# Performance work log

Hardware: AMD Instinct MI355X
Metric: run time of the kernel (lower is better)

## Reference

```python
import jax, jax.numpy as jnp
import numpy as np

N, E, T, S, R, L = 100000, 1600000, 4, 32, 16, 5
H = 3 * S  # out-head hidden (hidden_list=[n_scalars*3])
EPS = 1e-8


def _mlp(x, W1, b1, W2, b2):
    return jax.nn.silu(x @ W1 + b1) @ W2 + b2


def setup_inputs() -> dict:
    key = jax.random.key(0)
    ks = iter(jax.random.split(key, 40))
    rn = lambda *s: jax.random.normal(next(ks), s, dtype=jnp.float32)
    p = lambda *s: rn(*s) * 0.1
    inp = {
        'u': rn(N, T),
        'v': rn(N, T, 2),
        'boundary_norm': rn(N, 2),
        'is_boundary': jnp.zeros((N,), dtype=bool),
        'y_force': rn(N, 2),
        'pos': rn(N, 2),
        'edge_index': jax.random.randint(next(ks), (2, E), 0, N, dtype=jnp.int64),
        # node embedding MLP: invariant feats (2T+2) -> 2S -> S
        'Wn1': p(2 * T + 2, 2 * S), 'bn1': jnp.zeros((2 * S,)),
        'Wn2': p(2 * S, S), 'bn2': jnp.zeros((S,)),
        # L stacked InvBlock params: edge MLP (2S+R -> S -> S), node update (2S -> S -> S)
        'We1': p(L, 2 * S + R, S), 'be1': jnp.zeros((L, S)),
        'We2': p(L, S, S), 'be2': jnp.zeros((L, S)),
        'Wu1': p(L, 2 * S, S), 'bu1': jnp.zeros((L, S)),
        'Wu2': p(L, S, S), 'bu2': jnp.zeros((L, S)),
        'ln_g': jnp.ones((S,)), 'ln_b': jnp.zeros((S,)),
        # heads: S -> 3S -> {2,1}
        'Wr1': p(S, H), 'br1': jnp.zeros((H,)), 'Wr2': p(H, 2), 'br2': jnp.zeros((2,)),
        'Ws1': p(S, H), 'bs1': jnp.zeros((H,)), 'Ws2': p(H, 1), 'bs2': jnp.zeros((1,)),
    }
    return inp


def _forward(u, v, boundary_norm, y_force, pos, edge_index,
             Wn1, bn1, Wn2, bn2, We1, be1, We2, be2, Wu1, bu1, Wu2, bu2,
             ln_g, ln_b, Wr1, br1, Wr2, br2, Ws1, bs1, Ws2, bs2):
    # torch.no_grad() geometry branch: center positions, edge distances
    posc = jax.lax.stop_gradient(pos - pos.mean(axis=0))
    row, col = edge_index[0], edge_index[1]
    edge_vec = posc[row] - posc[col]                       # [E,2]
    dist = jnp.linalg.norm(edge_vec, axis=1)               # [E]
    # besel_linspace(start=0, end=1, number=R, cutoff=False): Bessel/sine RBF
    freqs = jnp.arange(1, R + 1, dtype=jnp.float32) * jnp.pi
    rbf = jnp.sqrt(2.0) * jnp.sin(dist[:, None] * freqs) / (dist[:, None] + EPS)  # [E,R]

    # Node_embedding_inv: SE(2)-invariant scalar features -> MLP
    feats = jnp.concatenate([
        u,                                                 # [N,T]
        jnp.linalg.norm(v, axis=-1),                       # [N,T]
        jnp.linalg.norm(boundary_norm, axis=-1, keepdims=True),
        jnp.linalg.norm(y_force, axis=-1, keepdims=True),
    ], axis=-1)                                            # [N,2T+2]
    x = _mlp(feats, Wn1, bn1, Wn2, bn2)                    # [N,S]

    # degree for mean aggregation (computed once)
    deg = jax.ops.segment_sum(jnp.ones((E,), jnp.float32), row, num_segments=N)
    inv_deg = 1.0 / jnp.maximum(deg, 1.0)                  # [N]

    for l in range(L):  # InvBlock message passing
        ef = jnp.concatenate([x[row], x[col], rbf], axis=-1)   # [E,2S+R]
        m = _mlp(ef, We1[l], be1[l], We2[l], be2[l])           # [E,S]
        agg = jax.ops.segment_sum(m, row, num_segments=N) * inv_deg[:, None]
        x = x + _mlp(jnp.concatenate([x, agg], axis=-1), Wu1[l], bu1[l], Wu2[l], bu2[l])

    # LayerNorm
    mu = x.mean(axis=-1, keepdims=True)
    var = jnp.var(x, axis=-1, keepdims=True)
    x = (x - mu) * jax.lax.rsqrt(var + 1e-5) * ln_g + ln_b

    v_ = _mlp(x, Wr1, br1, Wr2, br2)                       # [N,2]
    u_ = _mlp(x, Ws1, bs1, Ws2, bs2)                       # [N,1]
    return u[:, -1] + u_[:, 0], v_ + v[:, -1, :]


def reference(u, v, boundary_norm, is_boundary, y_force, pos, edge_index,
              Wn1, bn1, Wn2, bn2, We1, be1, We2, be2, Wu1, bu1, Wu2, bu2,
              ln_g, ln_b, Wr1, br1, Wr2, br2, Ws1, bs1, Ws2, bs2):
    del is_boundary  # unused by the visible forward
    return _forward(u, v, boundary_norm, y_force, pos, edge_index,
                    Wn1, bn1, Wn2, bn2, We1, be1, We2, be2, Wu1, bu1, Wu2, bu2,
                    ln_g, ln_b, Wr1, br1, Wr2, br2, Ws1, bs1, Ws2, bs2)
```

## Files before the change

### kernel.cpp

```cpp
#include <hip/hip_runtime.h>
#include <cmath>

namespace {

constexpr int N = 100000;
constexpr int E = 1600000;
constexpr int S = 32;
constexpr int L = 5;
constexpr int NPW = 16;
constexpr int LB2 = (N + 63) / 64;
constexpr int NBKT = 391;
constexpr int EPB  = E / 256;
constexpr float PI_F    = 3.14159265358979323846f;
constexpr float SQRT2_F = 1.41421356237309515f;

typedef __attribute__((ext_vector_type(8))) short short8;
typedef __attribute__((ext_vector_type(4))) float f32x4;

__device__ __forceinline__ float silu_f(float x) {
    return x * __builtin_amdgcn_rcpf(1.0f + __expf(-x));
}

__device__ __forceinline__ unsigned short f2bf(float f) {
    unsigned int u = __float_as_uint(f);
    u = (u + 0x7FFFu + ((u >> 16) & 1u)) >> 16;
    return (unsigned short)u;
}

__device__ __forceinline__ int rl(int v, int i) {
    return __builtin_amdgcn_readlane(v, i);
}

__device__ __forceinline__ short8 ld_xb(const unsigned short* base, int col, int quad) {
    unsigned off = ((unsigned)col << 6) | ((unsigned)quad << 4);
    return *reinterpret_cast<const short8*>(reinterpret_cast<const char*>(base) + off);
}

__device__ __forceinline__ short8 ld_rbf(const unsigned short* base, int slot, int quad) {
    unsigned off = ((unsigned)slot << 5) | ((unsigned)quad << 4);
    return *reinterpret_cast<const short8*>(reinterpret_cast<const char*>(base) + off);
}

__device__ __forceinline__ void adv(int& i, int& t, int vd) {
    ++t;
    while (i < 16) {
        int dgi = rl(vd, i);
        int nt = (dgi + 15) >> 4;
        if (t < nt) break;
        t = 0; ++i;
    }
}

__device__ __forceinline__ int slotOf(int i, int t, int vs, int vd, int ml) {
    if (i >= 16) return 0;
    int s0 = rl(vs, i);
    int dg = rl(vd, i);
    int smax = s0 + ((dg > 0) ? dg : 1) - 1;
    int s = s0 + t * 16 + ml;
    return min(s, smax);
}

__global__ __launch_bounds__(1024) void passA_kernel(
    const int* __restrict__ ei, int* __restrict__ hist)
{
    __shared__ int h[NBKT];
    int t = threadIdx.x;
    int blk = blockIdx.x;
    for (int b = t; b < NBKT; b += 1024) h[b] = 0;
    __syncthreads();
    int base = blk * EPB;
    for (int i = t; i < EPB; i += 1024) {
        int r = ei[base + i];
        atomicAdd(&h[r >> 8], 1);
    }
    __syncthreads();
    for (int b = t; b < NBKT; b += 1024) hist[b * 256 + blk] = h[b];
}

__global__ __launch_bounds__(512) void p1_kernel(
    const int* __restrict__ hist, int* __restrict__ bstart)
{
    __shared__ int tot[512];
    int t = threadIdx.x;
    int wv = t >> 6;
    int lane = t & 63;

    for (int bin = wv; bin < NBKT; bin += 8) {
        const int* row = hist + bin * 256;
        int s = row[lane] + row[lane + 64] + row[lane + 128] + row[lane + 192];
        s += __shfl_xor(s, 1, 64);
        s += __shfl_xor(s, 2, 64);
        s += __shfl_xor(s, 4, 64);
        s += __shfl_xor(s, 8, 64);
        s += __shfl_xor(s, 16, 64);
        s += __shfl_xor(s, 32, 64);
        if (lane == 0) tot[bin] = s;
    }
    __syncthreads();

    if (t >= NBKT) tot[t] = 0;
    __syncthreads();
    #pragma unroll
    for (int off = 1; off < 512; off <<= 1) {
        int v = (t >= off) ? tot[t - off] : 0;
        __syncthreads();
        tot[t] += v;
        __syncthreads();
    }
    if (t <= NBKT) bstart[t] = (t == 0) ? 0 : tot[t - 1];
}

__global__ __launch_bounds__(256) void p2_kernel(
    const int* __restrict__ hist, const int* __restrict__ bstart,
    int* __restrict__ base)
{
    __shared__ int pre[256];
    int t = threadIdx.x;
    int bin = blockIdx.x;
    int h = hist[bin * 256 + t];
    pre[t] = h;
    __syncthreads();
    #pragma unroll
    for (int off = 1; off < 256; off <<= 1) {
        int v = (t >= off) ? pre[t - off] : 0;
        __syncthreads();
        pre[t] += v;
        __syncthreads();
    }
    base[bin * 256 + t] = bstart[bin] + pre[t] - h;
}

__global__ __launch_bounds__(1024) void passB_kernel(
    const int* __restrict__ ei, const float* __restrict__ pos,
    const int* __restrict__ base, uint4* __restrict__ edgebuf)
{
    __shared__ int cur[NBKT];
    int t = threadIdx.x;
    int blk = blockIdx.x;
    for (int b = t; b < NBKT; b += 1024) cur[b] = base[b * 256 + blk];
    __syncthreads();
    int ebase = blk * EPB;
    for (int i = t; i < EPB; i += 1024) {
        int e = ebase + i;
        int r = ei[e];
        int c = ei[E + e];
        float2 pr = reinterpret_cast<const float2*>(pos)[r];
        float2 pc = reinterpret_cast<const float2*>(pos)[c];
        float dx = pr.x - pc.x, dy = pr.y - pc.y;
        float d = sqrtf(dx * dx + dy * dy);
        int slot = atomicAdd(&cur[r >> 8], 1);
        edgebuf[slot] = make_uint4((unsigned)c, __float_as_uint(d), (unsigned)r, 0u);
    }
}

__global__ __launch_bounds__(1024) void passC_kernel(
    const uint4* __restrict__ edgebuf, const int* __restrict__ bstart,
    int* __restrict__ deg, int* __restrict__ start,
    int* __restrict__ csr_col, unsigned short* __restrict__ rbf_buf)
{
    __shared__ int cnt[256];
    __shared__ int pre[256];
    __shared__ int cur[256];
    int t = threadIdx.x;
    int bkt = blockIdx.x;
    int s0 = bstart[bkt], s1 = bstart[bkt + 1];

    if (t < 256) cnt[t] = 0;
    __syncthreads();
    for (int i = s0 + t; i < s1; i += 1024) {
        unsigned r = edgebuf[i].z;
        atomicAdd(&cnt[r & 255], 1);
    }
    __syncthreads();
    int c0 = 0;
    if (t < 256) {
        c0 = cnt[t];
        pre[t] = c0;
    }
    __syncthreads();
    #pragma unroll
    for (int off = 1; off < 256; off <<= 1) {
        int v = 0;
        if (t < 256) v = (t >= off) ? pre[t - off] : 0;
        __syncthreads();
        if (t < 256) pre[t] += v;
        __syncthreads();
    }
    if (t < 256) {
        int row = bkt * 256 + t;
        int st = s0 + pre[t] - c0;
        if (row < N) {
            deg[row] = c0;
            start[row] = st;
        }
        cur[t] = st;
    }
    __syncthreads();

    for (int i = s0 + t; i < s1; i += 1024) {
        uint4 e = edgebuf[i];
        int slot = atomicAdd(&cur[e.z & 255], 1);
        csr_col[slot] = (int)e.x;
        float d = __uint_as_float(e.y);

        float sn = __sinf(PI_F * d);
        float c1 = __cosf(PI_F * d);
        float inv = SQRT2_F / (d + 1e-8f);
        float tc = 2.0f * c1;
        float sk = sn, skm = 0.0f;
        unsigned int pk[8];
        #pragma unroll
        for (int k = 0; k < 8; ++k) {
            float r0 = sk * inv;
            float s2 = tc * sk - skm; skm = sk; sk = s2;
            float r1 = sk * inv;
            float s3 = tc * sk - skm; skm = sk; sk = s3;
            pk[k] = (unsigned int)f2bf(r0) | ((unsigned int)f2bf(r1) << 16);
        }
        uint4* out = reinterpret_cast<uint4*>(rbf_buf + (size_t)slot * 16);
        out[0] = make_uint4(pk[0], pk[1], pk[2], pk[3]);
        out[1] = make_uint4(pk[4], pk[5], pk[6], pk[7]);
    }
}

__global__ __launch_bounds__(256) void prep_wt_kernel(
    const float* __restrict__ We1, const float* __restrict__ We2,
    const float* __restrict__ Wu1, const float* __restrict__ Wu2,
    const float* __restrict__ Wr1, const float* __restrict__ Ws1,
    const float* __restrict__ Wn2,
    short* __restrict__ wt1, short* __restrict__ wt2,
    short* __restrict__ wtu1, short* __restrict__ wtu2,
    short* __restrict__ wtr1, short* __restrict__ wts1,
    short* __restrict__ wtn2)
{
    int idx = blockIdx.x * 256 + threadIdx.x;
    if (idx < 5 * 32 * 96) {
        int l = idx / (32 * 96), r = idx % (32 * 96), n = r / 96, k = r % 96;
        float v = (k < 80) ? We1[((size_t)l * 80 + k) * 32 + n] : 0.0f;
        wt1[idx] = (short)f2bf(v);
    }
    if (idx < 5 * 32 * 32) {
        int l = idx / 1024, r = idx % 1024, n = r / 32, k = r % 32;
        wt2[idx]  = (short)f2bf(We2[((size_t)l * 32 + k) * 32 + n]);
        wtu2[idx] = (short)f2bf(Wu2[((size_t)l * 32 + k) * 32 + n]);
    }
    if (idx < 5 * 32 * 64) {
        int l = idx / 2048, r = idx % 2048, n = r / 64, k = r % 64;
        wtu1[idx] = (short)f2bf(Wu1[((size_t)l * 64 + k) * 32 + n]);
    }
    if (idx < 96 * 32) {
        int n = idx / 32, k = idx % 32;
        wtr1[idx] = (short)f2bf(Wr1[k * 96 + n]);
        wts1[idx] = (short)f2bf(Ws1[k * 96 + n]);
    }
    if (idx < 32 * 64) {
        int n = idx / 64, k = idx % 64;
        wtn2[idx] = (short)f2bf(Wn2[k * 32 + n]);
    }
}

__global__ __launch_bounds__(256) void node_embed_kernel(
    const float* __restrict__ u, const float* __restrict__ v,
    const float* __restrict__ bnorm, const float* __restrict__ yf,
    const float* __restrict__ Wn1, const float* __restrict__ bn1,
    const short* __restrict__ wtn2, const float* __restrict__ bn2,
    float* __restrict__ x, unsigned short* __restrict__ xb)
{
    __shared__ unsigned short hb[4][16 * 68];
    int t = threadIdx.x;
    int w = t >> 6;
    int lane = t & 63;
    int quad = lane >> 4;
    int ml = lane & 15;
    int wid = blockIdx.x * 4 + w;
    int nbase = __builtin_amdgcn_readfirstlane(wid * NPW);
    if (nbase >= N) return;

    int n = nbase + ml;

    float f[10];
    float4 uu = reinterpret_cast<const float4*>(u)[n];
    f[0] = uu.x; f[1] = uu.y; f[2] = uu.z; f[3] = uu.w;
    float4 v0 = reinterpret_cast<const float4*>(v)[2 * n];
    float4 v1 = reinterpret_cast<const float4*>(v)[2 * n + 1];
    f[4] = sqrtf(v0.x * v0.x + v0.y * v0.y);
    f[5] = sqrtf(v0.z * v0.z + v0.w * v0.w);
    f[6] = sqrtf(v1.x * v1.x + v1.y * v1.y);
    f[7] = sqrtf(v1.z * v1.z + v1.w * v1.w);
    float2 bb = reinterpret_cast<const float2*>(bnorm)[n];
    f[8] = sqrtf(bb.x * bb.x + bb.y * bb.y);
    float2 yy = reinterpret_cast<const float2*>(yf)[n];
    f[9] = sqrtf(yy.x * yy.x + yy.y * yy.y);

    float h[16];
    {
        const float4* b4 = reinterpret_cast<const float4*>(bn1 + quad * 16);
        float4 b0 = b4[0], b1 = b4[1], b2 = b4[2], b3 = b4[3];
        h[0]=b0.x; h[1]=b0.y; h[2]=b0.z; h[3]=b0.w;
        h[4]=b1.x; h[5]=b1.y; h[6]=b1.z; h[7]=b1.w;
        h[8]=b2.x; h[9]=b2.y; h[10]=b2.z; h[11]=b2.w;
        h[12]=b3.x; h[13]=b3.y; h[14]=b3.z; h[15]=b3.w;
    }
    #pragma unroll
    for (int i = 0; i < 10; ++i) {
        float ff = f[i];
        const float4* wr = reinterpret_cast<const float4*>(Wn1 + i * 64 + quad * 16);
        float4 w0 = wr[0], w1 = wr[1], w2 = wr[2], w3 = wr[3];
        h[0]  = fmaf(ff, w0.x, h[0]);  h[1]  = fmaf(ff, w0.y, h[1]);
        h[2]  = fmaf(ff, w0.z, h[2]);  h[3]  = fmaf(ff, w0.w, h[3]);
        h[4]  = fmaf(ff, w1.x, h[4]);  h[5]  = fmaf(ff, w1.y, h[5]);
        h[6]  = fmaf(ff, w1.z, h[6]);  h[7]  = fmaf(ff, w1.w, h[7]);
        h[8]  = fmaf(ff, w2.x, h[8]);  h[9]  = fmaf(ff, w2.y, h[9]);
        h[10] = fmaf(ff, w2.z, h[10]); h[11] = fmaf(ff, w2.w, h[11]);
        h[12] = fmaf(ff, w3.x, h[12]); h[13] = fmaf(ff, w3.y, h[13]);
        h[14] = fmaf(ff, w3.z, h[14]); h[15] = fmaf(ff, w3.w, h[15]);
    }
    #pragma unroll
    for (int jj = 0; jj < 16; ++jj) h[jj] = silu_f(h[jj]);

    unsigned short* hp = hb[w];
    {
        unsigned int* dst = reinterpret_cast<unsigned int*>(hp + ml * 68 + quad * 16);
        #pragma unroll
        for (int i = 0; i < 8; ++i)
            dst[i] = (unsigned int)f2bf(h[2 * i]) | ((unsigned int)f2bf(h[2 * i + 1]) << 16);
    }
    __builtin_amdgcn_wave_barrier();

    short8 Ak0 = *reinterpret_cast<const short8*>(hp + ml * 68 + quad * 8);
    short8 Ak1 = *reinterpret_cast<const short8*>(hp + ml * 68 + 32 + quad * 8);
    const short8* n2p = reinterpret_cast<const short8*>(wtn2);
    short8 B00 = n2p[(ml     ) * 8 + quad];
    short8 B01 = n2p[(ml     ) * 8 + 4 + quad];
    short8 B10 = n2p[(ml + 16) * 8 + quad];
    short8 B11 = n2p[(ml + 16) * 8 + 4 + quad];
    float bz0 = bn2[ml], bz1 = bn2[ml + 16];
    f32x4 a0 = {bz0, bz0, bz0, bz0};
    f32x4 a1 = {bz1, bz1, bz1, bz1};
    a0 = __builtin_amdgcn_mfma_f32_16x16x32_bf16(Ak0, B00, a0, 0, 0, 0);
    a0 = __builtin_amdgcn_mfma_f32_16x16x32_bf16(Ak1, B01, a0, 0, 0, 0);
    a1 = __builtin_amdgcn_mfma_f32_16x16x32_bf16(Ak0, B10, a1, 0, 0, 0);
    a1 = __builtin_amdgcn_mfma_f32_16x16x32_bf16(Ak1, B11, a1, 0, 0, 0);

    int row = quad * 4;
    #pragma unroll
    for (int r = 0; r < 4; ++r) {
        int nn = nbase + row + r;
        float o0 = a0[r];
        float o1 = a1[r];
        x[(size_t)nn * 32 + ml]      = o0;
        x[(size_t)nn * 32 + ml + 16] = o1;
        xb[(size_t)nn * 32 + ml]      = f2bf(o0);
        xb[(size_t)nn * 32 + ml + 16] = f2bf(o1);
    }
}

__global__ __launch_bounds__(256, 6) void layer_kernel(
    const int* __restrict__ deg, const int* __restrict__ start,
    const int* __restrict__ csr_col, const unsigned short* __restrict__ rbf_buf,
    const float* __restrict__ x_in, const unsigned short* __restrict__ xb_in,
    float* __restrict__ x_out, unsigned short* __restrict__ xb_out,
    const short* __restrict__ wt1, const float* __restrict__ b1,
    const short* __restrict__ wt2, const float* __restrict__ b2,
    const short* __restrict__ wtu1, const float* __restrict__ bu1,
    const short* __restrict__ wtu2, const float* __restrict__ bu2)
{
    __shared__ unsigned short lsh[4][16 * 34];
    __shared__ unsigned short agb[4][16 * 34];
    __shared__ unsigned short hub[4][16 * 34];
    __shared__ float lrp[4][16 * 33];
    __shared__ float ldg[4][16];
    __shared__ float livd[4][16];

    int t = threadIdx.x;
    int w = t >> 6;
    int lane = t & 63;
    int quad = lane >> 4;
    int ml = lane & 15;
    int wid = blockIdx.x * 4 + w;
    int nbase = __builtin_amdgcn_readfirstlane(wid * NPW);
    if (nbase >= N) return;

    int vs = start[nbase + ml];
    int vd = deg[nbase + ml];

    const short8* wp = reinterpret_cast<const short8*>(wt1);
    short8 B00 = wp[(ml     ) * 12 + 0 * 4 + quad];
    short8 B01 = wp[(ml     ) * 12 + 1 * 4 + quad];
    short8 B02 = wp[(ml     ) * 12 + 2 * 4 + quad];
    short8 B10 = wp[(ml + 16) * 12 + 0 * 4 + quad];
    short8 B11 = wp[(ml + 16) * 12 + 1 * 4 + quad];
    short8 B12 = wp[(ml + 16) * 12 + 2 * 4 + quad];

    short8 Ax = ld_xb(xb_in, nbase + ml, quad);

    float b1j0 = b1[ml];
    float b1j1 = b1[ml + 16];

    unsigned short* lshp = lsh[w];
    for (int k = lane; k < 16 * 34; k += 64) lshp[k] = 0;
    if (lane < 16) {
        ldg[w][lane] = (float)vd;
        livd[w][lane] = 1.0f / fmaxf((float)vd, 1.0f);
    }

    float* rpp = lrp[w];
    {
        f32x4 rp0 = {b1j0, b1j0, b1j0, b1j0};
        f32x4 rp1 = {b1j1, b1j1, b1j1, b1j1};
        rp0 = __builtin_amdgcn_mfma_f32_16x16x32_bf16(Ax, B00, rp0, 0, 0, 0);
        rp1 = __builtin_amdgcn_mfma_f32_16x16x32_bf16(Ax, B10, rp1, 0, 0, 0);
        int row = quad * 4;
        #pragma unroll
        for (int r = 0; r < 4; ++r) {
            rpp[(row + r) * 33 + ml]      = rp0[r];
            rpp[(row + r) * 33 + ml + 16] = rp1[r];
        }
    }
    __builtin_amdgcn_wave_barrier();

    const short8 Z8 = {0, 0, 0, 0, 0, 0, 0, 0};
    int iA = 0, tA = -1; adv(iA, tA, vd);
    int iB = iA, tB = tA; adv(iB, tB, vd);
    int iC = iB, tC = tB; adv(iC, tC, vd);
    int iD = iC, tD = tC; adv(iD, tD, vd);
    int iE = iD, tE = tD; adv(iE, tE, vd);

    int slot0 = slotOf(iA, tA, vs, vd, ml);
    int slot1 = slotOf(iB, tB, vs, vd, ml);
    int slot2 = slotOf(iC, tC, vs, vd, ml);
    int slotQ = slotOf(iD, tD, vs, vd, ml);
    int col0 = csr_col[slot0];
    int col1 = csr_col[slot1];
    int col2 = csr_col[slot2];
    int colQ = csr_col[slotQ];

    short8 F1_0 = ld_xb(xb_in, col0, quad);
    short8 F2_0 = (quad < 2) ? ld_rbf(rbf_buf, slot0, quad) : Z8;
    short8 F1_1 = ld_xb(xb_in, col1, quad);
    short8 F2_1 = (quad < 2) ? ld_rbf(rbf_buf, slot1, quad) : Z8;
    short8 F1_2 = ld_xb(xb_in, col2, quad);
    short8 F2_2 = (quad < 2) ? ld_rbf(rbf_buf, slot2, quad) : Z8;

    float colp0 = 0.0f, colp1 = 0.0f;

    auto tile = [&](const short8& A1, const short8& A2) {
        float rpa = rpp[iA * 33 + ml];
        float rpb = rpp[iA * 33 + ml + 16];
        f32x4 acc0 = {rpa, rpa, rpa, rpa};
        f32x4 acc1 = {rpb, rpb, rpb, rpb};
        acc0 = __builtin_amdgcn_mfma_f32_16x16x32_bf16(A1, B01, acc0, 0, 0, 0);
        acc0 = __builtin_amdgcn_mfma_f32_16x16x32_bf16(A2, B02, acc0, 0, 0, 0);
        acc1 = __builtin_amdgcn_mfma_f32_16x16x32_bf16(A1, B11, acc1, 0, 0, 0);
        acc1 = __builtin_amdgcn_mfma_f32_16x16x32_bf16(A2, B12, acc1, 0, 0, 0);

        int dg0 = rl(vd, iA);
        int rowbase = tA * 16 + quad * 4;
        #pragma unroll
        for (int r = 0; r < 4; ++r) {
            bool vld = (rowbase + r) < dg0;
            colp0 += vld ? silu_f(acc0[r]) : 0.0f;
            colp1 += vld ? silu_f(acc1[r]) : 0.0f;
        }
        if (tA == ((dg0 + 15) >> 4) - 1) {
            colp0 += __shfl_xor(colp0, 16, 64);
            colp0 += __shfl_xor(colp0, 32, 64);
            colp1 += __shfl_xor(colp1, 16, 64);
            colp1 += __shfl_xor(colp1, 32, 64);
            if (quad == 0) {
                lshp[iA * 34 + ml]      = f2bf(colp0);
                lshp[iA * 34 + ml + 16] = f2bf(colp1);
            }
            colp0 = 0.0f; colp1 = 0.0f;
        }
    };
    auto shiftq = [&]() {
        iA = iB; tA = tB; iB = iC; tB = tC;
        iC = iD; tC = tD; iD = iE; tD = tE;
        adv(iE, tE, vd);
    };

    #define EDGE_STEP(F1s, F2s)                                     \
    {                                                               \
        int slotE_ = slotOf(iE, tE, vs, vd, ml);                    \
        int colE_  = csr_col[slotE_];                               \
        tile(F1s, F2s);                                             \
        F1s = ld_xb(xb_in, colQ, quad);                             \
        F2s = (quad < 2) ? ld_rbf(rbf_buf, slotQ, quad) : Z8;       \
        shiftq();                                                   \
        colQ = colE_; slotQ = slotE_;                               \
    }

    while (iA < 16) {
        EDGE_STEP(F1_0, F2_0);
        if (iA >= 16) break;
        EDGE_STEP(F1_1, F2_1);
        if (iA >= 16) break;
        EDGE_STEP(F1_2, F2_2);
    }
    #undef EDGE_STEP
    __builtin_amdgcn_wave_barrier();

    const short8* w2p = reinterpret_cast<const short8*>(wt2);
    short8 Bw2_0 = w2p[(ml     ) * 4 + quad];
    short8 Bw2_1 = w2p[(ml + 16) * 4 + quad];
    const short8* u1p = reinterpret_cast<const short8*>(wtu1);
    short8 Bu1_00 = u1p[(ml     ) * 8 + quad];
    short8 Bu1_10 = u1p[(ml     ) * 8 + 4 + quad];
    short8 Bu1_01 = u1p[(ml + 16) * 8 + quad];
    short8 Bu1_11 = u1p[(ml + 16) * 8 + 4 + quad];
    const short8* u2p = reinterpret_cast<const short8*>(wtu2);
    short8 Bu2_0 = u2p[(ml     ) * 4 + quad];
    short8 Bu2_1 = u2p[(ml + 16) * 4 + quad];

    short8 Ash = *reinterpret_cast<const short8*>(lshp + ml * 34 + quad * 8);
    f32x4 c0 = {0.0f, 0.0f, 0.0f, 0.0f};
    f32x4 c1 = {0.0f, 0.0f, 0.0f, 0.0f};
    c0 = __builtin_amdgcn_mfma_f32_16x16x32_bf16(Ash, Bw2_0, c0, 0, 0, 0);
    c1 = __builtin_amdgcn_mfma_f32_16x16x32_bf16(Ash, Bw2_1, c1, 0, 0, 0);
    float b2c0 = b2[ml], b2c1 = b2[ml + 16];
    unsigned short* agp = agb[w];
    int row = quad * 4;
    #pragma unroll
    for (int r = 0; r < 4; ++r) {
        float fd = ldg[w][row + r];
        float iv = livd[w][row + r];
        agp[(row + r) * 34 + ml]      = f2bf((c0[r] + fd * b2c0) * iv);
        agp[(row + r) * 34 + ml + 16] = f2bf((c1[r] + fd * b2c1) * iv);
    }
    __builtin_amdgcn_wave_barrier();

    short8 Aag = *reinterpret_cast<const short8*>(agp + ml * 34 + quad * 8);
    f32x4 d0 = {0.0f, 0.0f, 0.0f, 0.0f};
    f32x4 d1 = {0.0f, 0.0f, 0.0f, 0.0f};
    d0 = __builtin_amdgcn_mfma_f32_16x16x32_bf16(Ax,  Bu1_00, d0, 0, 0, 0);
    d0 = __builtin_amdgcn_mfma_f32_16x16x32_bf16(Aag, Bu1_10, d0, 0, 0, 0);
    d1 = __builtin_amdgcn_mfma_f32_16x16x32_bf16(Ax,  Bu1_01, d1, 0, 0, 0);
    d1 = __builtin_amdgcn_mfma_f32_16x16x32_bf16(Aag, Bu1_11, d1, 0, 0, 0);
    float bu1c0 = bu1[ml], bu1c1 = bu1[ml + 16];
    unsigned short* hup = hub[w];
    #pragma unroll
    for (int r = 0; r < 4; ++r) {
        hup[(row + r) * 34 + ml]      = f2bf(silu_f(d0[r] + bu1c0));
        hup[(row + r) * 34 + ml + 16] = f2bf(silu_f(d1[r] + bu1c1));
    }
    __builtin_amdgcn_wave_barrier();

    short8 Ahu = *reinterpret_cast<const short8*>(hup + ml * 34 + quad * 8);
    float xr0[4], xr1[4];
    #pragma unroll
    for (int r = 0; r < 4; ++r) {
        int nn = nbase + row + r;
        xr0[r] = x_in[(size_t)nn * 32 + ml];
        xr1[r] = x_in[(size_t)nn * 32 + ml + 16];
    }
    f32x4 e0 = {0.0f, 0.0f, 0.0f, 0.0f};
    f32x4 e1 = {0.0f, 0.0f, 0.0f, 0.0f};
    e0 = __builtin_amdgcn_mfma_f32_16x16x32_bf16(Ahu, Bu2_0, e0, 0, 0, 0);
    e1 = __builtin_amdgcn_mfma_f32_16x16x32_bf16(Ahu, Bu2_1, e1, 0, 0, 0);
    float bu2c0 = bu2[ml], bu2c1 = bu2[ml + 16];
    #pragma unroll
    for (int r = 0; r < 4; ++r) {
        int nn = nbase + row + r;
        float o0 = e0[r] + bu2c0 + xr0[r];
        float o1 = e1[r] + bu2c1 + xr1[r];
        x_out[(size_t)nn * 32 + ml]      = o0;
        x_out[(size_t)nn * 32 + ml + 16] = o1;
        xb_out[(size_t)nn * 32 + ml]      = f2bf(o0);
        xb_out[(size_t)nn * 32 + ml + 16] = f2bf(o1);
    }
}

__global__ __launch_bounds__(256) void final_kernel(
    const float* __restrict__ x, const float* __restrict__ u,
    const float* __restrict__ v,
    const float* __restrict__ ln_g, const float* __restrict__ ln_b,
    const short* __restrict__ wtr1, const float* __restrict__ br1,
    const float* __restrict__ Wr2, const float* __restrict__ br2,
    const short* __restrict__ wts1, const float* __restrict__ bs1,
    const float* __restrict__ Ws2, const float* __restrict__ bs2,
    float* __restrict__ out)
{
    int t = threadIdx.x;
    int w = t >> 6;
    int lane = t & 63;
    int quad = lane >> 4;
    int ml = lane & 15;
    int wid = blockIdx.x * 4 + w;
    int nbase = __builtin_amdgcn_readfirstlane(wid * NPW);
    if (nbase >= N) return;

    const float4* xs = reinterpret_cast<const float4*>(
        x + (size_t)(nbase + ml) * 32 + quad * 8);
    float4 xa = xs[0], xb4 = xs[1];
    float f[8] = {xa.x, xa.y, xa.z, xa.w, xb4.x, xb4.y, xb4.z, xb4.w};

    float s = 0.0f, ss = 0.0f;
    #pragma unroll
    for (int i = 0; i < 8; ++i) { s += f[i]; ss += f[i] * f[i]; }
    s  += __shfl_xor(s, 16, 64);  s  += __shfl_xor(s, 32, 64);
    ss += __shfl_xor(ss, 16, 64); ss += __shfl_xor(ss, 32, 64);
    float mu = s * (1.0f / 32.0f);
    float var = ss * (1.0f / 32.0f) - mu * mu;
    float rs = rsqrtf(var + 1e-5f);

    const float4* gp = reinterpret_cast<const float4*>(ln_g + quad * 8);
    const float4* bp = reinterpret_cast<const float4*>(ln_b + quad * 8);
    float4 g0 = gp[0], g1 = gp[1], bb0 = bp[0], bb1 = bp[1];
    float gg[8] = {g0.x, g0.y, g0.z, g0.w, g1.x, g1.y, g1.z, g1.w};
    float bb[8] = {bb0.x, bb0.y, bb0.z, bb0.w, bb1.x, bb1.y, bb1.z, bb1.w};
    short8 A;
    #pragma unroll
    for (int i = 0; i < 8; ++i)
        A[i] = (short)f2bf((f[i] - mu) * rs * gg[i] + bb[i]);

    const short8* r1p = reinterpret_cast<const short8*>(wtr1);
    const short8* s1p = reinterpret_cast<const short8*>(wts1);
    const f32x4 Zf = {0.0f, 0.0f, 0.0f, 0.0f};
    f32x4 hr[6], hs[6];
    #pragma unroll
    for (int h = 0; h < 6; ++h) {
        hr[h] = __builtin_amdgcn_mfma_f32_16x16x32_bf16(A, r1p[(ml + 16 * h) * 4 + quad], Zf, 0, 0, 0);
        hs[h] = __builtin_amdgcn_mfma_f32_16x16x32_bf16(A, s1p[(ml + 16 * h) * 4 + quad], Zf, 0, 0, 0);
    }

    float wr2a[6], wr2b[6], ws2v[6], br1v[6], bs1v[6];
    #pragma unroll
    for (int h = 0; h < 6; ++h) {
        int j = ml + 16 * h;
        float2 wr = reinterpret_cast<const float2*>(Wr2)[j];
        wr2a[h] = wr.x; wr2b[h] = wr.y;
        ws2v[h] = Ws2[j];
        br1v[h] = br1[j];
        bs1v[h] = bs1[j];
    }

    float o0[4], o1[4], o2[4];
    #pragma unroll
    for (int r = 0; r < 4; ++r) {
        float p0 = 0.0f, p1 = 0.0f, p2 = 0.0f;
        #pragma unroll
        for (int h = 0; h < 6; ++h) {
            float a1 = silu_f(hr[h][r] + br1v[h]);
            float a2 = silu_f(hs[h][r] + bs1v[h]);
            p0 = fmaf(a1, wr2a[h], p0);
            p1 = fmaf(a1, wr2b[h], p1);
            p2 = fmaf(a2, ws2v[h], p2);
        }
        p0 += __shfl_xor(p0, 1, 64); p0 += __shfl_xor(p0, 2, 64);
        p0 += __shfl_xor(p0, 4, 64); p0 += __shfl_xor(p0, 8, 64);
        p1 += __shfl_xor(p1, 1, 64); p1 += __shfl_xor(p1, 2, 64);
        p1 += __shfl_xor(p1, 4, 64); p1 += __shfl_xor(p1, 8, 64);
        p2 += __shfl_xor(p2, 1, 64); p2 += __shfl_xor(p2, 2, 64);
        p2 += __shfl_xor(p2, 4, 64); p2 += __shfl_xor(p2, 8, 64);
        o0[r] = p0; o1[r] = p1; o2[r] = p2;
    }

    if (ml == 0) {
        float b20 = br2[0], b21 = br2[1], b22 = bs2[0];
        #pragma unroll
        for (int r = 0; r < 4; ++r) {
            int n = nbase + quad * 4 + r;
            out[n] = u[n * 4 + 3] + o2[r] + b22;
            out[N + 2 * n]     = o0[r] + b20 + v[n * 8 + 6];
            out[N + 2 * n + 1] = o1[r] + b21 + v[n * 8 + 7];
        }
    }
}

}

extern "C" void kernel_launch(void* const* d_in, const int* in_sizes, int n_in,
                              void* d_out, int out_size, void* d_ws, size_t ws_size,
                              hipStream_t stream)
{
    const float* u    = (const float*)d_in[0];
    const float* v    = (const float*)d_in[1];
    const float* bno  = (const float*)d_in[2];
    const float* yf   = (const float*)d_in[4];
    const float* pos  = (const float*)d_in[5];
    const int*   ei   = (const int*)d_in[6];
    const float* Wn1  = (const float*)d_in[7];
    const float* bn1  = (const float*)d_in[8];
    const float* Wn2  = (const float*)d_in[9];
    const float* bn2  = (const float*)d_in[10];
    const float* We1  = (const float*)d_in[11];
    const float* be1  = (const float*)d_in[12];
    const float* We2  = (const float*)d_in[13];
    const float* be2  = (const float*)d_in[14];
    const float* Wu1  = (const float*)d_in[15];
    const float* bu1  = (const float*)d_in[16];
    const float* Wu2  = (const float*)d_in[17];
    const float* bu2  = (const float*)d_in[18];
    const float* ln_g = (const float*)d_in[19];
    const float* ln_b = (const float*)d_in[20];
    const float* Wr1  = (const float*)d_in[21];
    const float* br1  = (const float*)d_in[22];
    const float* Wr2  = (const float*)d_in[23];
    const float* br2  = (const float*)d_in[24];
    const float* Ws1  = (const float*)d_in[25];
    const float* bs1  = (const float*)d_in[26];
    const float* Ws2  = (const float*)d_in[27];
    const float* bs2  = (const float*)d_in[28];
    float* out = (float*)d_out;

    int*   deg      = (int*)d_ws;
    int*   start    = deg + N;
    int*   bstart   = start + N;
    int*   csr_col  = bstart + 512;
    unsigned short* rbf = (unsigned short*)(csr_col + E);
    float* x0       = (float*)(rbf + (size_t)E * 16);
    float* x1       = x0 + (size_t)N * S;
    unsigned short* xb0 = (unsigned short*)(x1 + (size_t)N * S);
    unsigned short* xb1 = xb0 + (size_t)N * S;
    short* wt1      = (short*)(xb1 + (size_t)N * S);
    short* wt2      = wt1 + 5 * 32 * 96;
    short* wtu1     = wt2 + 5 * 32 * 32;
    short* wtu2     = wtu1 + 5 * 32 * 64;
    short* wtr1     = wtu2 + 5 * 32 * 32;
    short* wts1     = wtr1 + 96 * 32;
    short* wtn2     = wts1 + 96 * 32;
    int*   hist     = (int*)(wtn2 + 32 * 64);
    int*   basem    = hist + NBKT * 256;

    uint4* edgebuf = (uint4*)x0;

    passA_kernel<<<256, 1024, 0, stream>>>(ei, hist);
    p1_kernel<<<1, 512, 0, stream>>>(hist, bstart);
    p2_kernel<<<NBKT, 256, 0, stream>>>(hist, bstart, basem);
    passB_kernel<<<256, 1024, 0, stream>>>(ei, pos, basem, edgebuf);
    passC_kernel<<<NBKT, 1024, 0, stream>>>(edgebuf, bstart, deg, start, csr_col, rbf);
    prep_wt_kernel<<<60, 256, 0, stream>>>(We1, We2, Wu1, Wu2, Wr1, Ws1, Wn2,
                                           wt1, wt2, wtu1, wtu2, wtr1, wts1, wtn2);

    node_embed_kernel<<<LB2, 256, 0, stream>>>(u, v, bno, yf, Wn1, bn1, wtn2, bn2,
                                               x0, xb0);

    float* xin = x0;  float* xout = x1;
    unsigned short* xbin = xb0;  unsigned short* xbout = xb1;
    for (int l = 0; l < L; ++l) {
        layer_kernel<<<LB2, 256, 0, stream>>>(
            deg, start, csr_col, rbf, xin, xbin, xout, xbout,
            wt1 + (size_t)l * 32 * 96,  be1 + (size_t)l * 32,
            wt2 + (size_t)l * 32 * 32,  be2 + (size_t)l * 32,
            wtu1 + (size_t)l * 32 * 64, bu1 + (size_t)l * 32,
            wtu2 + (size_t)l * 32 * 32, bu2 + (size_t)l * 32);
        float* tf = xin; xin = xout; xout = tf;
        unsigned short* tb = xbin; xbin = xbout; xbout = tb;
    }

    final_kernel<<<LB2, 256, 0, stream>>>(xin, u, v, ln_g, ln_b,
                                          wtr1, br1, Wr2, br2,
                                          wts1, bs1, Ws2, bs2, out);
}
```

Baseline: 481.4 us.

## Precompute per-wave edge tile descriptors once instead of scanning degrees each layer

```diff
diff --git a/kernel.cpp b/kernel.cpp
--- a/kernel.cpp
+++ b/kernel.cpp
@@ -9,6 +9,8 @@
 constexpr int L = 5;
 constexpr int NPW = 16;
 constexpr int LB2 = (N + 63) / 64;
+constexpr int NG  = N / 16;
+constexpr int MAXT = 48;
 constexpr int NBKT = 391;
 constexpr int EPB  = E / 256;
 constexpr float PI_F    = 3.14159265358979323846f;
@@ -27,10 +29,6 @@
     return (unsigned short)u;
 }
 
-__device__ __forceinline__ int rl(int v, int i) {
-    return __builtin_amdgcn_readlane(v, i);
-}
-
 __device__ __forceinline__ short8 ld_xb(const unsigned short* base, int col, int quad) {
     unsigned off = ((unsigned)col << 6) | ((unsigned)quad << 4);
     return *reinterpret_cast<const short8*>(reinterpret_cast<const char*>(base) + off);
@@ -39,25 +37,6 @@
 __device__ __forceinline__ short8 ld_rbf(const unsigned short* base, int slot, int quad) {
     unsigned off = ((unsigned)slot << 5) | ((unsigned)quad << 4);
     return *reinterpret_cast<const short8*>(reinterpret_cast<const char*>(base) + off);
-}
-
-__device__ __forceinline__ void adv(int& i, int& t, int vd) {
-    ++t;
-    while (i < 16) {
-        int dgi = rl(vd, i);
-        int nt = (dgi + 15) >> 4;
-        if (t < nt) break;
-        t = 0; ++i;
-    }
-}
-
-__device__ __forceinline__ int slotOf(int i, int t, int vs, int vd, int ml) {
-    if (i >= 16) return 0;
-    int s0 = rl(vs, i);
-    int dg = rl(vd, i);
-    int smax = s0 + ((dg > 0) ? dg : 1) - 1;
-    int s = s0 + t * 16 + ml;
-    return min(s, smax);
 }
 
 __global__ __launch_bounds__(1024) void passA_kernel(
@@ -223,6 +202,37 @@
     }
 }
 
+__global__ __launch_bounds__(256) void tiles_kernel(
+    const int* __restrict__ deg, const int* __restrict__ start,
+    int2* __restrict__ wdesc, int* __restrict__ gcnt)
+{
+    int t = threadIdx.x;
+    int w = t >> 6;
+    int lane = t & 63;
+    int g = blockIdx.x * 4 + w;
+    if (g >= NG) return;
+
+    int d = 0, s = 0;
+    if (lane < 16) {
+        d = deg[g * 16 + lane];
+        s = start[g * 16 + lane];
+    }
+    int nt = (d + 15) >> 4;
+    int pre = nt;
+    #pragma unroll
+    for (int off = 1; off < 16; off <<= 1) {
+        int v = __shfl_up(pre, off, 16);
+        if ((lane & 15) >= off) pre += v;
+    }
+    if (lane < 16) {
+        int o = pre - nt;
+        int2* base = wdesc + (size_t)g * MAXT;
+        for (int tt = 0; tt < nt; ++tt)
+            base[o + tt] = make_int2(s + tt * 16, lane | ((d - tt * 16) << 8));
+        if (lane == 15) gcnt[g] = pre;
+    }
+}
+
 __global__ __launch_bounds__(256) void prep_wt_kernel(
     const float* __restrict__ We1, const float* __restrict__ We2,
     const float* __restrict__ Wu1, const float* __restrict__ Wu2,
@@ -356,7 +366,8 @@
 }
 
 __global__ __launch_bounds__(256, 6) void layer_kernel(
-    const int* __restrict__ deg, const int* __restrict__ start,
+    const int* __restrict__ deg, const int2* __restrict__ wdesc,
+    const int* __restrict__ gcnt,
     const int* __restrict__ csr_col, const unsigned short* __restrict__ rbf_buf,
     const float* __restrict__ x_in, const unsigned short* __restrict__ xb_in,
     float* __restrict__ x_out, unsigned short* __restrict__ xb_out,
@@ -381,7 +392,6 @@
     int nbase = __builtin_amdgcn_readfirstlane(wid * NPW);
     if (nbase >= N) return;
 
-    int vs = start[nbase + ml];
     int vd = deg[nbase + ml];
 
     const short8* wp = reinterpret_cast<const short8*>(wt1);
@@ -420,85 +430,84 @@
     __builtin_amdgcn_wave_barrier();
 
     const short8 Z8 = {0, 0, 0, 0, 0, 0, 0, 0};
-    int iA = 0, tA = -1; adv(iA, tA, vd);
-    int iB = iA, tB = tA; adv(iB, tB, vd);
-    int iC = iB, tC = tB; adv(iC, tC, vd);
-    int iD = iC, tD = tC; adv(iD, tD, vd);
-    int iE = iD, tE = tD; adv(iE, tE, vd);
-
-    int slot0 = slotOf(iA, tA, vs, vd, ml);
-    int slot1 = slotOf(iB, tB, vs, vd, ml);
-    int slot2 = slotOf(iC, tC, vs, vd, ml);
-    int slotQ = slotOf(iD, tD, vs, vd, ml);
-    int col0 = csr_col[slot0];
-    int col1 = csr_col[slot1];
-    int col2 = csr_col[slot2];
-    int colQ = csr_col[slotQ];
-
-    short8 F1_0 = ld_xb(xb_in, col0, quad);
-    short8 F2_0 = (quad < 2) ? ld_rbf(rbf_buf, slot0, quad) : Z8;
-    short8 F1_1 = ld_xb(xb_in, col1, quad);
-    short8 F2_1 = (quad < 2) ? ld_rbf(rbf_buf, slot1, quad) : Z8;
-    short8 F1_2 = ld_xb(xb_in, col2, quad);
-    short8 F2_2 = (quad < 2) ? ld_rbf(rbf_buf, slot2, quad) : Z8;
+    int tcnt = gcnt[wid];
+    const int2* dp = wdesc + (size_t)wid * MAXT;
 
     float colp0 = 0.0f, colp1 = 0.0f;
 
-    auto tile = [&](const short8& A1, const short8& A2) {
-        float rpa = rpp[iA * 33 + ml];
-        float rpb = rpp[iA * 33 + ml + 16];
-        f32x4 acc0 = {rpa, rpa, rpa, rpa};
-        f32x4 acc1 = {rpb, rpb, rpb, rpb};
-        acc0 = __builtin_amdgcn_mfma_f32_16x16x32_bf16(A1, B01, acc0, 0, 0, 0);
-        acc0 = __builtin_amdgcn_mfma_f32_16x16x32_bf16(A2, B02, acc0, 0, 0, 0);
-        acc1 = __builtin_amdgcn_mfma_f32_16x16x32_bf16(A1, B11, acc1, 0, 0, 0);
-        acc1 = __builtin_amdgcn_mfma_f32_16x16x32_bf16(A2, B12, acc1, 0, 0, 0);
-
-        int dg0 = rl(vd, iA);
-        int rowbase = tA * 16 + quad * 4;
-        #pragma unroll
-        for (int r = 0; r < 4; ++r) {
-            bool vld = (rowbase + r) < dg0;
-            colp0 += vld ? silu_f(acc0[r]) : 0.0f;
-            colp1 += vld ? silu_f(acc1[r]) : 0.0f;
+    if (tcnt > 0) {
+        auto dread = [&](int k) { return dp[min(k, tcnt - 1)]; };
+        auto slotfor = [&](int2 d) {
+            int drem = d.y >> 8;
+            return min(d.x + ml, d.x + drem - 1);
+        };
+
+        int2 dA = dp[0];
+        int2 dB = dread(1);
+        int2 dC = dread(2);
+        int2 dQ = dread(3);
+        int sA = slotfor(dA), sB = slotfor(dB), sC = slotfor(dC);
+        int sQ = slotfor(dQ);
+        int cQ = csr_col[sQ];
+
+        short8 F1_0 = ld_xb(xb_in, csr_col[sA], quad);
+        short8 F2_0 = (quad < 2) ? ld_rbf(rbf_buf, sA, quad) : Z8;
+        short8 F1_1 = ld_xb(xb_in, csr_col[sB], quad);
+        short8 F2_1 = (quad < 2) ? ld_rbf(rbf_buf, sB, quad) : Z8;
+        short8 F1_2 = ld_xb(xb_in, csr_col[sC], quad);
+        short8 F2_2 = (quad < 2) ? ld_rbf(rbf_buf, sC, quad) : Z8;
+
+        int k = 0;
+
+        #define EDGE_STEP(F1s, F2s)                                       \
+        {                                                                 \
+            int2 dN = dread(k + 4);                                       \
+            int sN = slotfor(dN);                                         \
+            int cN = csr_col[sN];                                         \
+            int i_ = dA.y & 255;                                          \
+            int drem = dA.y >> 8;                                         \
+            float rpa = rpp[i_ * 33 + ml];                                \
+            float rpb = rpp[i_ * 33 + ml + 16];                           \
+            f32x4 acc0 = {rpa, rpa, rpa, rpa};                            \
+            f32x4 acc1 = {rpb, rpb, rpb, rpb};                            \
+            acc0 = __builtin_amdgcn_mfma_f32_16x16x32_bf16(F1s, B01, acc0, 0, 0, 0); \
+            acc0 = __builtin_amdgcn_mfma_f32_16x16x32_bf16(F2s, B02, acc0, 0, 0, 0); \
+            acc1 = __builtin_amdgcn_mfma_f32_16x16x32_bf16(F1s, B11, acc1, 0, 0, 0); \
+            acc1 = __builtin_amdgcn_mfma_f32_16x16x32_bf16(F2s, B12, acc1, 0, 0, 0); \
+            int rowbase = quad * 4;                                       \
+            _Pragma("unroll")                                             \
+            for (int r = 0; r < 4; ++r) {                                 \
+                bool vld = (rowbase + r) < drem;                          \
+                colp0 += vld ? silu_f(acc0[r]) : 0.0f;                    \
+                colp1 += vld ? silu_f(acc1[r]) : 0.0f;                    \
+            }                                                             \
+            if (drem <= 16) {                                             \
+                colp0 += __shfl_xor(colp0, 16, 64);                       \
+                colp0 += __shfl_xor(colp0, 32, 64);                       \
+                colp1 += __shfl_xor(colp1, 16, 64);                       \
+                colp1 += __shfl_xor(colp1, 32, 64);                       \
+                if (quad == 0) {                                          \
+                    lshp[i_ * 34 + ml]      = f2bf(colp0);                \
+                    lshp[i_ * 34 + ml + 16] = f2bf(colp1);                \
+                }                                                         \
+                colp0 = 0.0f; colp1 = 0.0f;                               \
+            }                                                             \
+            F1s = ld_xb(xb_in, cQ, quad);                                 \
+            F2s = (quad < 2) ? ld_rbf(rbf_buf, sQ, quad) : Z8;            \
+            dA = dB; dB = dC; dC = dQ; dQ = dN;                           \
+            cQ = cN; sQ = sN;                                             \
+            ++k;                                                          \
         }
-        if (tA == ((dg0 + 15) >> 4) - 1) {
-            colp0 += __shfl_xor(colp0, 16, 64);
-            colp0 += __shfl_xor(colp0, 32, 64);
-            colp1 += __shfl_xor(colp1, 16, 64);
-            colp1 += __shfl_xor(colp1, 32, 64);
-            if (quad == 0) {
-                lshp[iA * 34 + ml]      = f2bf(colp0);
-                lshp[iA * 34 + ml + 16] = f2bf(colp1);
-            }
-            colp0 = 0.0f; colp1 = 0.0f;
+
+        while (k < tcnt) {
+            EDGE_STEP(F1_0, F2_0);
+            if (k >= tcnt) break;
+            EDGE_STEP(F1_1, F2_1);
+            if (k >= tcnt) break;
+            EDGE_STEP(F1_2, F2_2);
         }
-    };
-    auto shiftq = [&]() {
-        iA = iB; tA = tB; iB = iC; tB = tC;
-        iC = iD; tC = tD; iD = iE; tD = tE;
-        adv(iE, tE, vd);
-    };
-
-    #define EDGE_STEP(F1s, F2s)                                     \
-    {                                                               \
-        int slotE_ = slotOf(iE, tE, vs, vd, ml);                    \
-        int colE_  = csr_col[slotE_];                               \
-        tile(F1s, F2s);                                             \
-        F1s = ld_xb(xb_in, colQ, quad);                             \
-        F2s = (quad < 2) ? ld_rbf(rbf_buf, slotQ, quad) : Z8;       \
-        shiftq();                                                   \
-        colQ = colE_; slotQ = slotE_;                               \
-    }
-
-    while (iA < 16) {
-        EDGE_STEP(F1_0, F2_0);
-        if (iA >= 16) break;
-        EDGE_STEP(F1_1, F2_1);
-        if (iA >= 16) break;
-        EDGE_STEP(F1_2, F2_2);
-    }
-    #undef EDGE_STEP
+        #undef EDGE_STEP
+    }
     __builtin_amdgcn_wave_barrier();
 
     const short8* w2p = reinterpret_cast<const short8*>(wt2);
@@ -722,6 +731,8 @@
     short* wtn2     = wts1 + 96 * 32;
     int*   hist     = (int*)(wtn2 + 32 * 64);
     int*   basem    = hist + NBKT * 256;
+    int2*  wdesc    = (int2*)(basem + NBKT * 256);
+    int*   gcnt     = (int*)(wdesc + (size_t)NG * MAXT);
 
     uint4* edgebuf = (uint4*)x0;
 
@@ -730,6 +741,7 @@
     p2_kernel<<<NBKT, 256, 0, stream>>>(hist, bstart, basem);
     passB_kernel<<<256, 1024, 0, stream>>>(ei, pos, basem, edgebuf);
     passC_kernel<<<NBKT, 1024, 0, stream>>>(edgebuf, bstart, deg, start, csr_col, rbf);
+    tiles_kernel<<<LB2, 256, 0, stream>>>(deg, start, wdesc, gcnt);
     prep_wt_kernel<<<60, 256, 0, stream>>>(We1, We2, Wu1, Wu2, Wr1, Ws1, Wn2,
                                            wt1, wt2, wtu1, wtu2, wtr1, wts1, wtn2);
 
@@ -740,7 +752,7 @@
     unsigned short* xbin = xb0;  unsigned short* xbout = xb1;
     for (int l = 0; l < L; ++l) {
         layer_kernel<<<LB2, 256, 0, stream>>>(
-            deg, start, csr_col, rbf, xin, xbin, xout, xbout,
+            deg, wdesc, gcnt, csr_col, rbf, xin, xbin, xout, xbout,
             wt1 + (size_t)l * 32 * 96,  be1 + (size_t)l * 32,
             wt2 + (size_t)l * 32 * 32,  be2 + (size_t)l * 32,
             wtu1 + (size_t)l * 32 * 64, bu1 + (size_t)l * 32,
```

Result: slower. 754.0 us (+56.6%).

## Process edge tiles in pairs with 32x32x16 MFMA instead of 16x16x32

Applied to the files above, without the earlier changes.

```diff
diff --git a/kernel.cpp b/kernel.cpp
--- a/kernel.cpp
+++ b/kernel.cpp
@@ -16,6 +16,7 @@
 
 typedef __attribute__((ext_vector_type(8))) short short8;
 typedef __attribute__((ext_vector_type(4))) float f32x4;
+typedef __attribute__((ext_vector_type(16))) float f32x16;
 
 __device__ __forceinline__ float silu_f(float x) {
     return x * __builtin_amdgcn_rcpf(1.0f + __expf(-x));
@@ -31,13 +32,13 @@
     return __builtin_amdgcn_readlane(v, i);
 }
 
-__device__ __forceinline__ short8 ld_xb(const unsigned short* base, int col, int quad) {
-    unsigned off = ((unsigned)col << 6) | ((unsigned)quad << 4);
+__device__ __forceinline__ short8 ld_xb(const unsigned short* base, int col, int q) {
+    unsigned off = ((unsigned)col << 6) | ((unsigned)q << 4);
     return *reinterpret_cast<const short8*>(reinterpret_cast<const char*>(base) + off);
 }
 
-__device__ __forceinline__ short8 ld_rbf(const unsigned short* base, int slot, int quad) {
-    unsigned off = ((unsigned)slot << 5) | ((unsigned)quad << 4);
+__device__ __forceinline__ short8 ld_rbf(const unsigned short* base, int slot, int q) {
+    unsigned off = ((unsigned)slot << 5) | ((unsigned)q << 4);
     return *reinterpret_cast<const short8*>(reinterpret_cast<const char*>(base) + off);
 }
 
@@ -51,12 +52,12 @@
     }
 }
 
-__device__ __forceinline__ int slotOf(int i, int t, int vs, int vd, int ml) {
+__device__ __forceinline__ int slotOf(int i, int t, int vs, int vd, int e) {
     if (i >= 16) return 0;
     int s0 = rl(vs, i);
     int dg = rl(vd, i);
     int smax = s0 + ((dg > 0) ? dg : 1) - 1;
-    int s = s0 + t * 16 + ml;
+    int s = s0 + t * 16 + e;
     return min(s, smax);
 }
 
@@ -377,6 +378,7 @@
     int lane = t & 63;
     int quad = lane >> 4;
     int ml = lane & 15;
+    int hi = lane >> 5;
     int wid = blockIdx.x * 4 + w;
     int nbase = __builtin_amdgcn_readfirstlane(wid * NPW);
     if (nbase >= N) return;
@@ -386,11 +388,12 @@
 
     const short8* wp = reinterpret_cast<const short8*>(wt1);
     short8 B00 = wp[(ml     ) * 12 + 0 * 4 + quad];
-    short8 B01 = wp[(ml     ) * 12 + 1 * 4 + quad];
-    short8 B02 = wp[(ml     ) * 12 + 2 * 4 + quad];
     short8 B10 = wp[(ml + 16) * 12 + 0 * 4 + quad];
-    short8 B11 = wp[(ml + 16) * 12 + 1 * 4 + quad];
-    short8 B12 = wp[(ml + 16) * 12 + 2 * 4 + quad];
+
+    int bn = lane & 31;
+    short8 Bx0 = *reinterpret_cast<const short8*>(wt1 + bn * 96 + 32 + hi * 8);
+    short8 Bx1 = *reinterpret_cast<const short8*>(wt1 + bn * 96 + 48 + hi * 8);
+    short8 Brb = *reinterpret_cast<const short8*>(wt1 + bn * 96 + 64 + hi * 8);
 
     short8 Ax = ld_xb(xb_in, nbase + ml, quad);
 
@@ -419,84 +422,117 @@
     }
     __builtin_amdgcn_wave_barrier();
 
-    const short8 Z8 = {0, 0, 0, 0, 0, 0, 0, 0};
-    int iA = 0, tA = -1; adv(iA, tA, vd);
-    int iB = iA, tB = tA; adv(iB, tB, vd);
-    int iC = iB, tC = tB; adv(iC, tC, vd);
-    int iD = iC, tD = tC; adv(iD, tD, vd);
-    int iE = iD, tE = tD; adv(iE, tE, vd);
-
-    int slot0 = slotOf(iA, tA, vs, vd, ml);
-    int slot1 = slotOf(iB, tB, vs, vd, ml);
-    int slot2 = slotOf(iC, tC, vs, vd, ml);
-    int slotQ = slotOf(iD, tD, vs, vd, ml);
-    int col0 = csr_col[slot0];
-    int col1 = csr_col[slot1];
-    int col2 = csr_col[slot2];
+    int ia0 = 0, ta0 = -1; adv(ia0, ta0, vd);
+    int ia1 = ia0, ta1 = ta0; adv(ia1, ta1, vd);
+    int ib0 = ia1, tb0 = ta1; adv(ib0, tb0, vd);
+    int ib1 = ib0, tb1 = tb0; adv(ib1, tb1, vd);
+    int ic0 = ib1, tc0 = tb1; adv(ic0, tc0, vd);
+    int ic1 = ic0, tc1 = tc0; adv(ic1, tc1, vd);
+    int id0 = ic1, td0 = tc1; adv(id0, td0, vd);
+    int id1 = id0, td1 = td0; adv(id1, td1, vd);
+    int ie0 = id1, te0 = td1; adv(ie0, te0, vd);
+    int ie1 = ie0, te1 = te0; adv(ie1, te1, vd);
+
+    auto slotPair = [&](int i0, int t0, int i1, int t1) {
+        int sa = slotOf(i0, t0, vs, vd, ml);
+        int sb = slotOf(i1, t1, vs, vd, ml);
+        return (lane & 16) ? sb : sa;
+    };
+
+    int slotA = slotPair(ia0, ta0, ia1, ta1);
+    int slotB = slotPair(ib0, tb0, ib1, tb1);
+    int slotC = slotPair(ic0, tc0, ic1, tc1);
+    int slotQ = slotPair(id0, td0, id1, td1);
+    int colA = csr_col[slotA];
+    int colB = csr_col[slotB];
+    int colC = csr_col[slotC];
     int colQ = csr_col[slotQ];
 
-    short8 F1_0 = ld_xb(xb_in, col0, quad);
-    short8 F2_0 = (quad < 2) ? ld_rbf(rbf_buf, slot0, quad) : Z8;
-    short8 F1_1 = ld_xb(xb_in, col1, quad);
-    short8 F2_1 = (quad < 2) ? ld_rbf(rbf_buf, slot1, quad) : Z8;
-    short8 F1_2 = ld_xb(xb_in, col2, quad);
-    short8 F2_2 = (quad < 2) ? ld_rbf(rbf_buf, slot2, quad) : Z8;
-
-    float colp0 = 0.0f, colp1 = 0.0f;
-
-    auto tile = [&](const short8& A1, const short8& A2) {
-        float rpa = rpp[iA * 33 + ml];
-        float rpb = rpp[iA * 33 + ml + 16];
-        f32x4 acc0 = {rpa, rpa, rpa, rpa};
-        f32x4 acc1 = {rpb, rpb, rpb, rpb};
-        acc0 = __builtin_amdgcn_mfma_f32_16x16x32_bf16(A1, B01, acc0, 0, 0, 0);
-        acc0 = __builtin_amdgcn_mfma_f32_16x16x32_bf16(A2, B02, acc0, 0, 0, 0);
-        acc1 = __builtin_amdgcn_mfma_f32_16x16x32_bf16(A1, B11, acc1, 0, 0, 0);
-        acc1 = __builtin_amdgcn_mfma_f32_16x16x32_bf16(A2, B12, acc1, 0, 0, 0);
-
-        int dg0 = rl(vd, iA);
-        int rowbase = tA * 16 + quad * 4;
+    short8 X0_0 = ld_xb(xb_in, colA, hi);
+    short8 X1_0 = ld_xb(xb_in, colA, 2 + hi);
+    short8 RB_0 = ld_rbf(rbf_buf, slotA, hi);
+    short8 X0_1 = ld_xb(xb_in, colB, hi);
+    short8 X1_1 = ld_xb(xb_in, colB, 2 + hi);
+    short8 RB_1 = ld_rbf(rbf_buf, slotB, hi);
+    short8 X0_2 = ld_xb(xb_in, colC, hi);
+    short8 X1_2 = ld_xb(xb_in, colC, 2 + hi);
+    short8 RB_2 = ld_rbf(rbf_buf, slotC, hi);
+
+    float colp = 0.0f;
+
+    auto tilePair = [&](const short8& X0, const short8& X1, const short8& RB) {
+        int col = lane & 31;
+        float rpa = rpp[ia0 * 33 + col];
+        float rpb = (ia1 < 16) ? rpp[ia1 * 33 + col] : 0.0f;
+        f32x16 acc;
         #pragma unroll
-        for (int r = 0; r < 4; ++r) {
-            bool vld = (rowbase + r) < dg0;
-            colp0 += vld ? silu_f(acc0[r]) : 0.0f;
-            colp1 += vld ? silu_f(acc1[r]) : 0.0f;
+        for (int j = 0; j < 8; ++j)  acc[j] = rpa;
+        #pragma unroll
+        for (int j = 8; j < 16; ++j) acc[j] = rpb;
+        acc = __builtin_amdgcn_mfma_f32_32x32x16_bf16(X0, Bx0, acc, 0, 0, 0);
+        acc = __builtin_amdgcn_mfma_f32_32x32x16_bf16(X1, Bx1, acc, 0, 0, 0);
+        acc = __builtin_amdgcn_mfma_f32_32x32x16_bf16(RB, Brb, acc, 0, 0, 0);
+
+        int hi4 = hi * 4;
+        int dg0 = rl(vd, ia0);
+        int drem0 = dg0 - ta0 * 16;
+        float pa = 0.0f;
+        #pragma unroll
+        for (int j = 0; j < 8; ++j) {
+            int row = (j & 3) + 8 * (j >> 2) + hi4;
+            pa += (row < drem0) ? silu_f(acc[j]) : 0.0f;
         }
-        if (tA == ((dg0 + 15) >> 4) - 1) {
-            colp0 += __shfl_xor(colp0, 16, 64);
-            colp0 += __shfl_xor(colp0, 32, 64);
-            colp1 += __shfl_xor(colp1, 16, 64);
-            colp1 += __shfl_xor(colp1, 32, 64);
-            if (quad == 0) {
-                lshp[iA * 34 + ml]      = f2bf(colp0);
-                lshp[iA * 34 + ml + 16] = f2bf(colp1);
+        colp += pa;
+        if (ta0 == ((dg0 + 15) >> 4) - 1) {
+            float s2 = colp + __shfl_xor(colp, 32, 64);
+            if (lane < 32) lshp[ia0 * 34 + lane] = f2bf(s2);
+            colp = 0.0f;
+        }
+        if (ia1 < 16) {
+            int dg1 = rl(vd, ia1);
+            int drem1 = dg1 - ta1 * 16;
+            float pb = 0.0f;
+            #pragma unroll
+            for (int j = 8; j < 16; ++j) {
+                int row = (j & 3) + 8 * ((j >> 2) - 2) + hi4;
+                pb += (row < drem1) ? silu_f(acc[j]) : 0.0f;
             }
-            colp0 = 0.0f; colp1 = 0.0f;
+            colp += pb;
+            if (ta1 == ((dg1 + 15) >> 4) - 1) {
+                float s2 = colp + __shfl_xor(colp, 32, 64);
+                if (lane < 32) lshp[ia1 * 34 + lane] = f2bf(s2);
+                colp = 0.0f;
+            }
         }
     };
     auto shiftq = [&]() {
-        iA = iB; tA = tB; iB = iC; tB = tC;
-        iC = iD; tC = tD; iD = iE; tD = tE;
-        adv(iE, tE, vd);
+        ia0 = ib0; ta0 = tb0; ia1 = ib1; ta1 = tb1;
+        ib0 = ic0; tb0 = tc0; ib1 = ic1; tb1 = tc1;
+        ic0 = id0; tc0 = td0; ic1 = id1; tc1 = td1;
+        id0 = ie0; td0 = te0; id1 = ie1; td1 = te1;
+        int ni0 = ie1, nt0 = te1; adv(ni0, nt0, vd);
+        int ni1 = ni0, nt1 = nt0; adv(ni1, nt1, vd);
+        ie0 = ni0; te0 = nt0; ie1 = ni1; te1 = nt1;
     };
 
-    #define EDGE_STEP(F1s, F2s)                                     \
+    #define EDGE_STEP(X0s, X1s, RBs)                                \
     {                                                               \
-        int slotE_ = slotOf(iE, tE, vs, vd, ml);                    \
+        int slotE_ = slotPair(ie0, te0, ie1, te1);                  \
         int colE_  = csr_col[slotE_];                               \
-        tile(F1s, F2s);                                             \
-        F1s = ld_xb(xb_in, colQ, quad);                             \
-        F2s = (quad < 2) ? ld_rbf(rbf_buf, slotQ, quad) : Z8;       \
+        tilePair(X0s, X1s, RBs);                                    \
+        X0s = ld_xb(xb_in, colQ, hi);                               \
+        X1s = ld_xb(xb_in, colQ, 2 + hi);                           \
+        RBs = ld_rbf(rbf_buf, slotQ, hi);                           \
         shiftq();                                                   \
         colQ = colE_; slotQ = slotE_;                               \
     }
 
-    while (iA < 16) {
-        EDGE_STEP(F1_0, F2_0);
-        if (iA >= 16) break;
-        EDGE_STEP(F1_1, F2_1);
-        if (iA >= 16) break;
-        EDGE_STEP(F1_2, F2_2);
+    while (ia0 < 16) {
+        EDGE_STEP(X0_0, X1_0, RB_0);
+        if (ia0 >= 16) break;
+        EDGE_STEP(X0_1, X1_1, RB_1);
+        if (ia0 >= 16) break;
+        EDGE_STEP(X0_2, X1_2, RB_2);
     }
     #undef EDGE_STEP
     __builtin_amdgcn_wave_barrier();
```

Result: slower. 646.1 us (+34.2%).
